# Kernel tuning notes

Measured on AMD Instinct MI355X. Metric: run time of the kernel, lower is better.

## Reference

```python
import jax, jax.numpy as jnp
import numpy as np

B, N, C, H = 2, 2048, 512, 8
D = C // H
SCALE = D ** (-0.5)


def setup_inputs() -> dict:
    key = jax.random.key(0)
    k1, k2, k3 = jax.random.split(key, 3)
    x = jax.random.normal(k1, (B, N, C), dtype=jnp.float32)
    qkv_w = jax.random.normal(k2, (C, 3 * C), dtype=jnp.float32) * (C ** -0.5)
    proj_w = jax.random.normal(k3, (C, C), dtype=jnp.float32) * (C ** -0.5)
    proj_b = jnp.zeros((C,), dtype=jnp.float32)
    return {"x": x, "qkv_w": qkv_w, "proj_w": proj_w, "proj_b": proj_b}


def reference(x, qkv_w, proj_w, proj_b):
    # qkv projection (no bias) -> (B, N, 3, H, D) -> (3, B, H, N, D)
    qkv = jnp.einsum('bnc,cf->bnf', x, qkv_w)
    qkv = qkv.reshape(B, N, 3, H, D).transpose(2, 0, 3, 1, 4)
    q, k, v = qkv[0], qkv[1], qkv[2]
    q = q * SCALE
    attn = jnp.einsum('bhid,bhjd->bhij', q, k)          # (B, H, N, N)
    attn = jax.nn.softmax(attn, axis=-1)
    out = jnp.einsum('bhij,bhjd->bhid', attn, v)         # (B, H, N, D)
    # Faithful to source: reshape (B,H,N,D) -> (B,N,C) WITHOUT transposing
    out = out.reshape(B, N, C)
    out = jnp.einsum('bnc,cd->bnd', out, proj_w) + proj_b
    return out
```

## Files before the change

kernel.cpp:

```cpp
#include <hip/hip_runtime.h>
#include <math.h>

constexpr int Bb = 2;
constexpr int Nn = 2048;
constexpr int Cc = 512;
constexpr int Hh = 8;
constexpr int Dd = 64;

typedef short short8 __attribute__((ext_vector_type(8)));
typedef float floatx4 __attribute__((ext_vector_type(4)));
typedef float floatx16 __attribute__((ext_vector_type(16)));

__device__ inline short8 bcs8(uint4 u) { return __builtin_bit_cast(short8, u); }

__device__ inline floatx4 mfma16(short8 a, short8 b, floatx4 c) {
    return __builtin_amdgcn_mfma_f32_16x16x32_bf16(a, b, c, 0, 0, 0);
}
__device__ inline floatx16 mfma32(short8 a, short8 b, floatx16 c) {
    return __builtin_amdgcn_mfma_f32_32x32x16_bf16(a, b, c, 0, 0, 0);
}

#if __has_builtin(__builtin_amdgcn_exp2f)
#define EXP2(x) __builtin_amdgcn_exp2f(x)
#else
#define EXP2(x) __expf((x) * 0.69314718056f)
#endif

__device__ inline unsigned pk_trunc(float a, float b) {
    return __builtin_amdgcn_perm(__float_as_uint(b), __float_as_uint(a), 0x07060302u);
}
__device__ inline unsigned pk_rne(float a, float b) {
    unsigned ua = __float_as_uint(a); ua += 0x7fffu + ((ua >> 16) & 1u);
    unsigned ub = __float_as_uint(b); ub += 0x7fffu + ((ub >> 16) & 1u);
    return __builtin_amdgcn_perm(ub, ua, 0x07060302u);
}
__device__ inline unsigned short rne1(float a) {
    unsigned u = __float_as_uint(a); u += 0x7fffu + ((u >> 16) & 1u);
    return (unsigned short)(u >> 16);
}
__device__ inline float tr16(float a) {
    return __uint_as_float(__float_as_uint(a) & 0xffff0000u);
}
__device__ inline void split8(float4 A, float4 B, uint4& hi, uint4& lo) {
    hi = make_uint4(pk_trunc(A.x, A.y), pk_trunc(A.z, A.w),
                    pk_trunc(B.x, B.y), pk_trunc(B.z, B.w));
    lo = make_uint4(pk_trunc(A.x - tr16(A.x), A.y - tr16(A.y)),
                    pk_trunc(A.z - tr16(A.z), A.w - tr16(A.w)),
                    pk_trunc(B.x - tr16(B.x), B.y - tr16(B.y)),
                    pk_trunc(B.z - tr16(B.z), B.w - tr16(B.w)));
}


__global__ __launch_bounds__(256) void prep(const float* __restrict__ qkv_w,
                                            const float* __restrict__ proj_w,
                                            const float* __restrict__ x,
                                            unsigned short* __restrict__ wqfrag,
                                            unsigned short* __restrict__ wpfrag,
                                            unsigned short* __restrict__ xfrag)
{
    __shared__ float Tl[64][68];
    int bid = blockIdx.x;
    int t = threadIdx.x;
    if (bid >= 256) {
        int xb = bid - 256;
        int tok = xb * 16 + (t >> 4);
        int kc = t & 15;
        const float* px = x + (size_t)tok * 512 + kc * 32;
        uint4 h[4], l[4];
        #pragma unroll
        for (int o = 0; o < 4; ++o) {
            float4 fa = *(const float4*)(px + o * 8);
            float4 fb = *(const float4*)(px + o * 8 + 4);
            split8(fa, fb, h[o], l[o]);
        }
        int mt = tok >> 4, m = tok & 15;
        unsigned short* fb_ = xfrag + ((size_t)(mt * 16 + kc) * 2) * 512;
        #pragma unroll
        for (int o = 0; o < 4; ++o) {
            *(uint4*)(fb_ + (m + 16 * o) * 8) = h[o];
            *(uint4*)(fb_ + 512 + (m + 16 * o) * 8) = l[o];
        }
        return;
    }
    const float* src; unsigned short* dfrag; int W, f0, k0;
    if (bid < 192) { int kt = bid / 24, ft = bid % 24; W = 1536; src = qkv_w; dfrag = wqfrag; f0 = ft * 64; k0 = kt * 64; }
    else { int b2 = bid - 192; int kt = b2 / 8, ft = b2 % 8; W = 512; src = proj_w; dfrag = wpfrag; f0 = ft * 64; k0 = kt * 64; }
    {
        int kl = t >> 2, fc = (t & 3) * 16;
        const float* p = src + (size_t)(k0 + kl) * W + f0 + fc;
        #pragma unroll
        for (int i = 0; i < 4; ++i) {
            float4 v = *(const float4*)(p + i * 4);
            Tl[kl][fc + i * 4 + 0] = v.x; Tl[kl][fc + i * 4 + 1] = v.y;
            Tl[kl][fc + i * 4 + 2] = v.z; Tl[kl][fc + i * 4 + 3] = v.w;
        }
    }
    __syncthreads();
    {
        int fl = t >> 2, kc16 = (t & 3) * 16;
        float v[16];
        #pragma unroll
        for (int i = 0; i < 16; ++i) v[i] = Tl[kc16 + i][fl];
        unsigned hi[8], lo[8];
        #pragma unroll
        for (int i = 0; i < 8; ++i) {
            float a = v[2 * i], b = v[2 * i + 1];
            hi[i] = pk_trunc(a, b);
            lo[i] = pk_trunc(a - tr16(a), b - tr16(b));
        }
        int f = f0 + fl;
        int nt = f >> 4, nin = f & 15;
        int kc = (k0 + kc16) >> 5;
        int oct0 = (kc16 >> 3) & 3;
        unsigned short* fb_ = dfrag + ((size_t)(nt * 16 + kc) * 2) * 512;
        *(uint4*)(fb_ + (nin + 16 * oct0) * 8) = make_uint4(hi[0], hi[1], hi[2], hi[3]);
        *(uint4*)(fb_ + (nin + 16 * (oct0 + 1)) * 8) = make_uint4(hi[4], hi[5], hi[6], hi[7]);
        *(uint4*)(fb_ + 512 + (nin + 16 * oct0) * 8) = make_uint4(lo[0], lo[1], lo[2], lo[3]);
        *(uint4*)(fb_ + 512 + (nin + 16 * (oct0 + 1)) * 8) = make_uint4(lo[4], lo[5], lo[6], lo[7]);
    }
}

__global__ __launch_bounds__(256, 3) void gemm_qkv(const unsigned short* __restrict__ xfrag,
                                                   const unsigned short* __restrict__ wqfrag,
                                                   unsigned short* __restrict__ qd,
                                                   unsigned short* __restrict__ kfrag,
                                                   unsigned short* __restrict__ vfrag)
{
    const int tid = threadIdx.x, lane = tid & 63, w = tid >> 6;
    const int l15 = lane & 15, l4 = lane >> 4;
    const int row0 = blockIdx.y * 64, col0 = blockIdx.x * 128;
    const int mt0 = row0 >> 4;
    const int nt0 = (col0 >> 4) + w * 2;

    floatx4 acc[4][2];
    #pragma unroll
    for (int i = 0; i < 4; ++i)
        #pragma unroll
        for (int j = 0; j < 2; ++j)
            #pragma unroll
            for (int r = 0; r < 4; ++r) acc[i][j][r] = 0.f;

    const unsigned short* xb = xfrag + (size_t)lane * 8;
    const unsigned short* wb = wqfrag + (size_t)lane * 8;

    #pragma unroll
    for (int kc = 0; kc < 16; ++kc) {
        short8 bf[2][2];
        #pragma unroll
        for (int nt = 0; nt < 2; ++nt) {
            size_t fb_ = ((size_t)((nt0 + nt) * 16 + kc) * 2) * 512;
            bf[nt][0] = bcs8(*(const uint4*)(wb + fb_));
            bf[nt][1] = bcs8(*(const uint4*)(wb + fb_ + 512));
        }
        #pragma unroll
        for (int mt = 0; mt < 4; ++mt) {
            size_t fa_ = ((size_t)((mt0 + mt) * 16 + kc) * 2) * 512;
            short8 ah = bcs8(*(const uint4*)(xb + fa_));
            short8 al = bcs8(*(const uint4*)(xb + fa_ + 512));
            #pragma unroll
            for (int nt = 0; nt < 2; ++nt) {
                acc[mt][nt] = mfma16(ah, bf[nt][0], acc[mt][nt]);
                acc[mt][nt] = mfma16(ah, bf[nt][1], acc[mt][nt]);
                acc[mt][nt] = mfma16(al, bf[nt][0], acc[mt][nt]);
            }
        }
    }
    #pragma unroll
    for (int mt = 0; mt < 4; ++mt)
        #pragma unroll
        for (int nt = 0; nt < 2; ++nt) {
            int c = col0 + (w * 2 + nt) * 16 + l15;
            int which = c >> 9;
            int head = (c >> 6) & 7, d = c & 63;
            int tokb = row0 + mt * 16 + l4 * 4;
            int b = tokb >> 11, nn = tokb & 2047;
            int bh = b * 8 + head;
            if (which == 0) {
                #pragma unroll
                for (int r = 0; r < 4; ++r)
                    qd[(size_t)(bh * 2048 + nn + r) * 64 + d] = rne1(acc[mt][nt][r] * 0.18033688f);
            } else if (which == 1) {
                int s = d >> 4;
                size_t fb_ = ((size_t)(bh * 64 + (nn >> 5)) * 4 + s) * 512 + (d & 7);
                int hl = ((d >> 3) & 1) * 32;
                #pragma unroll
                for (int r = 0; r < 4; ++r)
                    kfrag[fb_ + (size_t)(hl + ((nn + r) & 31)) * 8] = rne1(acc[mt][nt][r]);
            } else {
                int j = nn >> 4, mtv = d >> 5;
                uint2 pv;
                pv.x = pk_rne(acc[mt][nt][0], acc[mt][nt][1]);
                pv.y = pk_rne(acc[mt][nt][2], acc[mt][nt][3]);
                *(uint2*)&vfrag[((size_t)(bh * 128 + j) * 2 + mtv) * 512 +
                                (size_t)(((nn >> 3) & 1) * 32 + (d & 31)) * 8 + (nn & 7)] = pv;
            }
        }
}

__global__ __launch_bounds__(256, 2) void attn(const unsigned short* __restrict__ qd,
                                               const unsigned short* __restrict__ kfrag,
                                               const unsigned short* __restrict__ vfrag,
                                               unsigned short* __restrict__ Ofrag)
{
    __shared__ float Pp[2][64][65];
    __shared__ float Lsp[2][64];

    int bid = blockIdx.x;
    int xcd = bid & 7; int rr = bid >> 3;
    int qt = rr & 31; int bhi = rr >> 5;
    int bh = (bhi << 3) | xcd;
    int tid = threadIdx.x, lane = tid & 63, kg = tid >> 6;
    int l31 = lane & 31, h = lane >> 5;

    short8 qf[2][4];
    #pragma unroll
    for (int qh = 0; qh < 2; ++qh)
        #pragma unroll
        for (int s = 0; s < 4; ++s)
            qf[qh][s] = bcs8(*(const uint4*)(qd + ((size_t)bh * 2048 + qt * 64 + qh * 32 + l31) * 64 + s * 16 + h * 8));

    const uint4 onesu = make_uint4(0x3F803F80u, 0x3F803F80u, 0x3F803F80u, 0x3F803F80u);
    const short8 onesf = bcs8(onesu);

    floatx16 OT[2][2], OTl[2];
    #pragma unroll
    for (int qh = 0; qh < 2; ++qh) {
        #pragma unroll
        for (int i = 0; i < 2; ++i)
            #pragma unroll
            for (int r = 0; r < 16; ++r) OT[qh][i][r] = 0.f;
        #pragma unroll
        for (int r = 0; r < 16; ++r) OTl[qh][r] = 0.f;
    }

    const unsigned short* kb_ = kfrag + ((size_t)(bh * 64 + kg * 16) * 4) * 512 + lane * 8;
    const unsigned short* vb_ = vfrag + ((size_t)(bh * 128 + kg * 32) * 2) * 512 + lane * 8;

    #pragma unroll
    for (int c = 0; c < 16; ++c) {
        uint4 kfu[4];
        #pragma unroll
        for (int s = 0; s < 4; ++s)
            kfu[s] = *(const uint4*)(kb_ + ((size_t)c * 4 + s) * 512);
        uint4 vfu[2][2];
        #pragma unroll
        for (int kc = 0; kc < 2; ++kc)
            #pragma unroll
            for (int mtv = 0; mtv < 2; ++mtv)
                vfu[kc][mtv] = *(const uint4*)(vb_ + ((size_t)(c * 2 + kc) * 2 + mtv) * 512);

        #pragma unroll
        for (int qh = 0; qh < 2; ++qh) {
            floatx16 st;
            #pragma unroll
            for (int r = 0; r < 16; ++r) st[r] = 0.f;
            #pragma unroll
            for (int s = 0; s < 4; ++s) st = mfma32(bcs8(kfu[s]), qf[qh][s], st);

            unsigned P2[8];
            #pragma unroll
            for (int s2 = 0; s2 < 8; ++s2)
                P2[s2] = pk_trunc(EXP2(st[2 * s2]), EXP2(st[2 * s2 + 1]));

            #pragma unroll
            for (int kc = 0; kc < 2; ++kc) {
                unsigned X0 = P2[4 * kc + 0], X1 = P2[4 * kc + 1];
                unsigned Y0 = P2[4 * kc + 2], Y1 = P2[4 * kc + 3];
                unsigned T0 = h ? X0 : Y0;
                unsigned T1 = h ? X1 : Y1;
                unsigned To0 = __shfl_xor(T0, 32, 64);
                unsigned To1 = __shfl_xor(T1, 32, 64);
                uint4 fu;
                fu.x = h ? To0 : X0;
                fu.y = h ? To1 : X1;
                fu.z = h ? Y0 : To0;
                fu.w = h ? Y1 : To1;
                short8 pf = bcs8(fu);
                OT[qh][0] = mfma32(bcs8(vfu[kc][0]), pf, OT[qh][0]);
                OT[qh][1] = mfma32(bcs8(vfu[kc][1]), pf, OT[qh][1]);
                OTl[qh] = mfma32(onesf, pf, OTl[qh]);
            }
        }
    }

    if (kg < 2) {
        #pragma unroll
        for (int qh = 0; qh < 2; ++qh) {
            int q = qh * 32 + l31;
            #pragma unroll
            for (int mtv = 0; mtv < 2; ++mtv)
                #pragma unroll
                for (int r = 0; r < 16; ++r) {
                    int d = mtv * 32 + (r & 3) + 8 * (r >> 2) + 4 * h;
                    Pp[kg][q][d] = OT[qh][mtv][r];
                }
            Lsp[kg][q] = OTl[qh][0];
        }
    }
    __syncthreads();
    if (kg >= 2) {
        #pragma unroll
        for (int qh = 0; qh < 2; ++qh) {
            int q = qh * 32 + l31;
            #pragma unroll
            for (int mtv = 0; mtv < 2; ++mtv)
                #pragma unroll
                for (int r = 0; r < 16; ++r) {
                    int d = mtv * 32 + (r & 3) + 8 * (r >> 2) + 4 * h;
                    Pp[kg - 2][q][d] += OT[qh][mtv][r];
                }
            if (h == 0) Lsp[kg - 2][q] += OTl[qh][0];
        }
    }
    __syncthreads();
    {
        int q = tid >> 2, dc = (tid & 3) * 16;
        float linv = 1.f / (Lsp[0][q] + Lsp[1][q]);
        float vv[16];
        #pragma unroll
        for (int i = 0; i < 16; ++i)
            vv[i] = (Pp[0][q][dc + i] + Pp[1][q][dc + i]) * linv;
        unsigned hi[8], lo[8];
        #pragma unroll
        for (int i = 0; i < 8; ++i) {
            float a = vv[2 * i], bb = vv[2 * i + 1];
            hi[i] = pk_trunc(a, bb);
            lo[i] = pk_trunc(a - tr16(a), bb - tr16(bb));
        }
        int ng = qt * 64 + q;
        int r = bh * 256 + (ng >> 3);
        int mt = r >> 4, m = r & 15;
        #pragma unroll
        for (int hh = 0; hh < 2; ++hh) {
            int cc = (ng & 7) * 64 + dc + hh * 8;
            int kc = cc >> 5, oct = (cc >> 3) & 3;
            unsigned short* fb_ = Ofrag + ((size_t)(mt * 16 + kc) * 2) * 512 + (m + 16 * oct) * 8;
            *(uint4*)fb_ = make_uint4(hi[4 * hh + 0], hi[4 * hh + 1], hi[4 * hh + 2], hi[4 * hh + 3]);
            *(uint4*)(fb_ + 512) = make_uint4(lo[4 * hh + 0], lo[4 * hh + 1], lo[4 * hh + 2], lo[4 * hh + 3]);
        }
    }
}

__global__ __launch_bounds__(256, 2) void gemm_proj(const unsigned short* __restrict__ Ofrag,
                                                    const unsigned short* __restrict__ wpfrag,
                                                    const float* __restrict__ bias,
                                                    float* __restrict__ out)
{
    const int tid = threadIdx.x, lane = tid & 63, w = tid >> 6;
    const int l15 = lane & 15, l4 = lane >> 4;
    const int row0 = blockIdx.y * 64, col0 = blockIdx.x * 64;
    const int wm = w >> 1, wn = w & 1;
    const int mt0 = (row0 >> 4) + wm * 2;
    const int nt0 = (col0 >> 4) + wn * 2;

    floatx4 acc[2][2];
    #pragma unroll
    for (int i = 0; i < 2; ++i)
        #pragma unroll
        for (int j = 0; j < 2; ++j)
            #pragma unroll
            for (int r = 0; r < 4; ++r) acc[i][j][r] = 0.f;

    const unsigned short* ab = Ofrag + (size_t)lane * 8;
    const unsigned short* wb = wpfrag + (size_t)lane * 8;

    #pragma unroll
    for (int kc = 0; kc < 16; ++kc) {
        short8 bf[2][2];
        #pragma unroll
        for (int nt = 0; nt < 2; ++nt) {
            size_t fb_ = ((size_t)((nt0 + nt) * 16 + kc) * 2) * 512;
            bf[nt][0] = bcs8(*(const uint4*)(wb + fb_));
            bf[nt][1] = bcs8(*(const uint4*)(wb + fb_ + 512));
        }
        #pragma unroll
        for (int mt = 0; mt < 2; ++mt) {
            size_t fa_ = ((size_t)((mt0 + mt) * 16 + kc) * 2) * 512;
            short8 ah = bcs8(*(const uint4*)(ab + fa_));
            short8 al = bcs8(*(const uint4*)(ab + fa_ + 512));
            #pragma unroll
            for (int nt = 0; nt < 2; ++nt) {
                acc[mt][nt] = mfma16(ah, bf[nt][0], acc[mt][nt]);
                acc[mt][nt] = mfma16(ah, bf[nt][1], acc[mt][nt]);
                acc[mt][nt] = mfma16(al, bf[nt][0], acc[mt][nt]);
            }
        }
    }
    #pragma unroll
    for (int mt = 0; mt < 2; ++mt)
        #pragma unroll
        for (int nt = 0; nt < 2; ++nt) {
            int c = col0 + wn * 32 + nt * 16 + l15;
            float bv = bias[c];
            #pragma unroll
            for (int r = 0; r < 4; ++r) {
                int tok = row0 + wm * 32 + mt * 16 + l4 * 4 + r;
                out[(size_t)tok * 512 + c] = acc[mt][nt][r] + bv;
            }
        }
}

extern "C" void kernel_launch(void* const* d_in, const int* in_sizes, int n_in,
                              void* d_out, int out_size, void* d_ws, size_t ws_size,
                              hipStream_t stream)
{
    const float* x      = (const float*)d_in[0];
    const float* qkv_w  = (const float*)d_in[1];
    const float* proj_w = (const float*)d_in[2];
    const float* proj_b = (const float*)d_in[3];
    float* out = (float*)d_out;

    char* ws = (char*)d_ws;
    unsigned short* xfrag  = (unsigned short*)ws;
    unsigned short* wqfrag = (unsigned short*)(ws + 8388608);
    unsigned short* wpfrag = (unsigned short*)(ws + 11534336);
    unsigned short* qd     = (unsigned short*)(ws + 12582912);
    unsigned short* kfrag  = (unsigned short*)(ws + 16777216);
    unsigned short* vfrag  = (unsigned short*)(ws + 20971520);
    unsigned short* Ofrag  = (unsigned short*)(ws + 25165824);

    prep<<<512, 256, 0, stream>>>(qkv_w, proj_w, x, wqfrag, wpfrag, xfrag);
    gemm_qkv<<<dim3(12, 64), 256, 0, stream>>>(xfrag, wqfrag, qd, kfrag, vfrag);
    attn<<<512, 256, 0, stream>>>(qd, kfrag, vfrag, Ofrag);
    gemm_proj<<<dim3(8, 64), 256, 0, stream>>>(Ofrag, wpfrag, proj_b, out);
}
```

Baseline: 136.5 us.

## Fuse attention and output projection into one kernel with flag-based sync

Merges the attention kernel and the projection GEMM into a single launch. Each block finishes its attention tile, writes O fragments, and publishes completion through per-(head, row-slab) atomic counters. It then spin-waits until the eight attention blocks that produce its projection row slab are done, and computes a 64x64 projection tile. This removes one kernel launch and the tail gap between the two kernels. The cost is spin-waiting, which depends on all 512 blocks being co-resident (2 per CU) to avoid deadlock, plus reliance on the workspace being large enough for the flags.

Measured after the change: 219.1 us. 1.6x slower.

```diff
diff --git a/kernel.cpp b/kernel.cpp
--- a/kernel.cpp
+++ b/kernel.cpp
@@ -56,11 +56,13 @@
                                             const float* __restrict__ x,
                                             unsigned short* __restrict__ wqfrag,
                                             unsigned short* __restrict__ wpfrag,
-                                            unsigned short* __restrict__ xfrag)
+                                            unsigned short* __restrict__ xfrag,
+                                            int* flags)
 {
     __shared__ float Tl[64][68];
     int bid = blockIdx.x;
     int t = threadIdx.x;
+    if (flags && bid == 0 && t < 64) flags[t] = 0;
     if (bid >= 256) {
         int xb = bid - 256;
         int tok = xb * 16 + (t >> 4);
@@ -195,6 +197,228 @@
                                 (size_t)(((nn >> 3) & 1) * 32 + (d & 31)) * 8 + (nn & 7)] = pv;
             }
         }
+}
+
+__global__ __launch_bounds__(256, 2) void attn_proj(const unsigned short* __restrict__ qd,
+                                                    const unsigned short* __restrict__ kfrag,
+                                                    const unsigned short* __restrict__ vfrag,
+                                                    unsigned short* __restrict__ Ofrag,
+                                                    const unsigned short* __restrict__ wpfrag,
+                                                    const float* __restrict__ bias,
+                                                    float* __restrict__ out,
+                                                    int* flags)
+{
+    __shared__ float Pp[2][64][65];
+    __shared__ float Lsp[2][64];
+
+    int bid = blockIdx.x;
+    int xcd = bid & 7; int rr = bid >> 3;
+    int qt = rr & 31; int bhi = rr >> 5;
+    int bh = (bhi << 3) | xcd;
+    int tid = threadIdx.x, lane = tid & 63, kg = tid >> 6;
+    int l31 = lane & 31, h = lane >> 5;
+
+    {
+        short8 qf[2][4];
+        #pragma unroll
+        for (int qh = 0; qh < 2; ++qh)
+            #pragma unroll
+            for (int s = 0; s < 4; ++s)
+                qf[qh][s] = bcs8(*(const uint4*)(qd + ((size_t)bh * 2048 + qt * 64 + qh * 32 + l31) * 64 + s * 16 + h * 8));
+
+        const uint4 onesu = make_uint4(0x3F803F80u, 0x3F803F80u, 0x3F803F80u, 0x3F803F80u);
+        const short8 onesf = bcs8(onesu);
+
+        floatx16 OT[2][2], OTl[2];
+        #pragma unroll
+        for (int qh = 0; qh < 2; ++qh) {
+            #pragma unroll
+            for (int i = 0; i < 2; ++i)
+                #pragma unroll
+                for (int r = 0; r < 16; ++r) OT[qh][i][r] = 0.f;
+            #pragma unroll
+            for (int r = 0; r < 16; ++r) OTl[qh][r] = 0.f;
+        }
+
+        const unsigned short* kb_ = kfrag + ((size_t)(bh * 64 + kg * 16) * 4) * 512 + lane * 8;
+        const unsigned short* vb_ = vfrag + ((size_t)(bh * 128 + kg * 32) * 2) * 512 + lane * 8;
+
+        #pragma unroll
+        for (int c = 0; c < 16; ++c) {
+            uint4 kfu[4];
+            #pragma unroll
+            for (int s = 0; s < 4; ++s)
+                kfu[s] = *(const uint4*)(kb_ + ((size_t)c * 4 + s) * 512);
+            uint4 vfu[2][2];
+            #pragma unroll
+            for (int kc = 0; kc < 2; ++kc)
+                #pragma unroll
+                for (int mtv = 0; mtv < 2; ++mtv)
+                    vfu[kc][mtv] = *(const uint4*)(vb_ + ((size_t)(c * 2 + kc) * 2 + mtv) * 512);
+
+            #pragma unroll
+            for (int qh = 0; qh < 2; ++qh) {
+                floatx16 st;
+                #pragma unroll
+                for (int r = 0; r < 16; ++r) st[r] = 0.f;
+                #pragma unroll
+                for (int s = 0; s < 4; ++s) st = mfma32(bcs8(kfu[s]), qf[qh][s], st);
+
+                unsigned P2[8];
+                #pragma unroll
+                for (int s2 = 0; s2 < 8; ++s2)
+                    P2[s2] = pk_trunc(EXP2(st[2 * s2]), EXP2(st[2 * s2 + 1]));
+
+                #pragma unroll
+                for (int kc = 0; kc < 2; ++kc) {
+                    unsigned X0 = P2[4 * kc + 0], X1 = P2[4 * kc + 1];
+                    unsigned Y0 = P2[4 * kc + 2], Y1 = P2[4 * kc + 3];
+                    unsigned T0 = h ? X0 : Y0;
+                    unsigned T1 = h ? X1 : Y1;
+                    unsigned To0 = __shfl_xor(T0, 32, 64);
+                    unsigned To1 = __shfl_xor(T1, 32, 64);
+                    uint4 fu;
+                    fu.x = h ? To0 : X0;
+                    fu.y = h ? To1 : X1;
+                    fu.z = h ? Y0 : To0;
+                    fu.w = h ? Y1 : To1;
+                    short8 pf = bcs8(fu);
+                    OT[qh][0] = mfma32(bcs8(vfu[kc][0]), pf, OT[qh][0]);
+                    OT[qh][1] = mfma32(bcs8(vfu[kc][1]), pf, OT[qh][1]);
+                    OTl[qh] = mfma32(onesf, pf, OTl[qh]);
+                }
+            }
+        }
+
+        if (kg < 2) {
+            #pragma unroll
+            for (int qh = 0; qh < 2; ++qh) {
+                int q = qh * 32 + l31;
+                #pragma unroll
+                for (int mtv = 0; mtv < 2; ++mtv)
+                    #pragma unroll
+                    for (int r = 0; r < 16; ++r) {
+                        int d = mtv * 32 + (r & 3) + 8 * (r >> 2) + 4 * h;
+                        Pp[kg][q][d] = OT[qh][mtv][r];
+                    }
+                Lsp[kg][q] = OTl[qh][0];
+            }
+        }
+        __syncthreads();
+        if (kg >= 2) {
+            #pragma unroll
+            for (int qh = 0; qh < 2; ++qh) {
+                int q = qh * 32 + l31;
+                #pragma unroll
+                for (int mtv = 0; mtv < 2; ++mtv)
+                    #pragma unroll
+                    for (int r = 0; r < 16; ++r) {
+                        int d = mtv * 32 + (r & 3) + 8 * (r >> 2) + 4 * h;
+                        Pp[kg - 2][q][d] += OT[qh][mtv][r];
+                    }
+                if (h == 0) Lsp[kg - 2][q] += OTl[qh][0];
+            }
+        }
+        __syncthreads();
+        {
+            int q = tid >> 2, dc = (tid & 3) * 16;
+            float linv = 1.f / (Lsp[0][q] + Lsp[1][q]);
+            float vv[16];
+            #pragma unroll
+            for (int i = 0; i < 16; ++i)
+                vv[i] = (Pp[0][q][dc + i] + Pp[1][q][dc + i]) * linv;
+            unsigned hi[8], lo[8];
+            #pragma unroll
+            for (int i = 0; i < 8; ++i) {
+                float a = vv[2 * i], bb = vv[2 * i + 1];
+                hi[i] = pk_trunc(a, bb);
+                lo[i] = pk_trunc(a - tr16(a), bb - tr16(bb));
+            }
+            int ng = qt * 64 + q;
+            int r = bh * 256 + (ng >> 3);
+            int mt = r >> 4, m = r & 15;
+            #pragma unroll
+            for (int hh = 0; hh < 2; ++hh) {
+                int cc = (ng & 7) * 64 + dc + hh * 8;
+                int kc = cc >> 5, oct = (cc >> 3) & 3;
+                unsigned short* fb_ = Ofrag + ((size_t)(mt * 16 + kc) * 2) * 512 + (m + 16 * oct) * 8;
+                *(uint4*)fb_ = make_uint4(hi[4 * hh + 0], hi[4 * hh + 1], hi[4 * hh + 2], hi[4 * hh + 3]);
+                *(uint4*)(fb_ + 512) = make_uint4(lo[4 * hh + 0], lo[4 * hh + 1], lo[4 * hh + 2], lo[4 * hh + 3]);
+            }
+        }
+    }
+
+    __syncthreads();
+    __threadfence();
+    if (tid == 0)
+        __hip_atomic_fetch_add(&flags[bh * 4 + (qt >> 3)], 1,
+                               __ATOMIC_RELEASE, __HIP_MEMORY_SCOPE_AGENT);
+
+    {
+        const int pbid = bid;
+        const int pbh = ((pbid >> 8) << 3) | (pbid & 7);
+        const int ps  = (pbid >> 6) & 3;
+        const int pbx = (pbid >> 3) & 7;
+        if (tid == 0) {
+            while (__hip_atomic_load(&flags[pbh * 4 + ps],
+                                     __ATOMIC_ACQUIRE, __HIP_MEMORY_SCOPE_AGENT) < 8)
+                __builtin_amdgcn_s_sleep(2);
+        }
+        __syncthreads();
+
+        const int row0 = pbh * 256 + ps * 64, col0 = pbx * 64;
+        const int w = tid >> 6;
+        const int l15 = lane & 15, l4 = lane >> 4;
+        const int wm = w >> 1, wn = w & 1;
+        const int mt0 = (row0 >> 4) + wm * 2;
+        const int nt0 = (col0 >> 4) + wn * 2;
+
+        floatx4 acc[2][2];
+        #pragma unroll
+        for (int i = 0; i < 2; ++i)
+            #pragma unroll
+            for (int j = 0; j < 2; ++j)
+                #pragma unroll
+                for (int r = 0; r < 4; ++r) acc[i][j][r] = 0.f;
+
+        const unsigned short* ab = Ofrag + (size_t)lane * 8;
+        const unsigned short* wb = wpfrag + (size_t)lane * 8;
+
+        #pragma unroll
+        for (int kc = 0; kc < 16; ++kc) {
+            short8 bf[2][2];
+            #pragma unroll
+            for (int nt = 0; nt < 2; ++nt) {
+                size_t fb_ = ((size_t)((nt0 + nt) * 16 + kc) * 2) * 512;
+                bf[nt][0] = bcs8(*(const uint4*)(wb + fb_));
+                bf[nt][1] = bcs8(*(const uint4*)(wb + fb_ + 512));
+            }
+            #pragma unroll
+            for (int mt = 0; mt < 2; ++mt) {
+                size_t fa_ = ((size_t)((mt0 + mt) * 16 + kc) * 2) * 512;
+                short8 ah = bcs8(*(const uint4*)(ab + fa_));
+                short8 al = bcs8(*(const uint4*)(ab + fa_ + 512));
+                #pragma unroll
+                for (int nt = 0; nt < 2; ++nt) {
+                    acc[mt][nt] = mfma16(ah, bf[nt][0], acc[mt][nt]);
+                    acc[mt][nt] = mfma16(ah, bf[nt][1], acc[mt][nt]);
+                    acc[mt][nt] = mfma16(al, bf[nt][0], acc[mt][nt]);
+                }
+            }
+        }
+        #pragma unroll
+        for (int mt = 0; mt < 2; ++mt)
+            #pragma unroll
+            for (int nt = 0; nt < 2; ++nt) {
+                int c = col0 + wn * 32 + nt * 16 + l15;
+                float bv = bias[c];
+                #pragma unroll
+                for (int r = 0; r < 4; ++r) {
+                    int tok = row0 + wm * 32 + mt * 16 + l4 * 4 + r;
+                    out[(size_t)tok * 512 + c] = acc[mt][nt][r] + bv;
+                }
+            }
+    }
 }
 
 __global__ __launch_bounds__(256, 2) void attn(const unsigned short* __restrict__ qd,
@@ -418,9 +642,14 @@
     unsigned short* kfrag  = (unsigned short*)(ws + 16777216);
     unsigned short* vfrag  = (unsigned short*)(ws + 20971520);
     unsigned short* Ofrag  = (unsigned short*)(ws + 25165824);
-
-    prep<<<512, 256, 0, stream>>>(qkv_w, proj_w, x, wqfrag, wpfrag, xfrag);
+    int* flags = (ws_size >= 33554432 + 256) ? (int*)(ws + 33554432) : nullptr;
+
+    prep<<<512, 256, 0, stream>>>(qkv_w, proj_w, x, wqfrag, wpfrag, xfrag, flags);
     gemm_qkv<<<dim3(12, 64), 256, 0, stream>>>(xfrag, wqfrag, qd, kfrag, vfrag);
-    attn<<<512, 256, 0, stream>>>(qd, kfrag, vfrag, Ofrag);
-    gemm_proj<<<dim3(8, 64), 256, 0, stream>>>(Ofrag, wpfrag, proj_b, out);
-}
+    if (flags) {
+        attn_proj<<<512, 256, 0, stream>>>(qd, kfrag, vfrag, Ofrag, wpfrag, proj_b, out, flags);
+    } else {
+        attn<<<512, 256, 0, stream>>>(qd, kfrag, vfrag, Ofrag);
+        gemm_proj<<<dim3(8, 64), 256, 0, stream>>>(Ofrag, wpfrag, proj_b, out);
+    }
+}
```
